# Kernel optimization log

Measured on AMD Instinct MI355X. Metric: run time of the kernel, lower is better.

## Reference

```python
import jax, jax.numpy as jnp
import numpy as np

B, T, C = 2, 2048, 1024
NH = 16
HD = C // NH

def build_alibi_bias(n_head, max_len):
    slopes = jnp.arange(1, n_head + 1, dtype=jnp.float32) / n_head  # [nh]
    ar = jnp.arange(max_len, dtype=jnp.float32)
    # bias[h, i, j] = slopes[h] * (j - i)
    return slopes[:, None, None] * (ar[None, None, :] - ar[None, :, None])

def setup_inputs() -> dict:
    key = jax.random.key(0)
    ks = jax.random.split(key, 7)
    s = 0.02
    return {
        "x": jax.random.normal(ks[0], (B, T, C), dtype=jnp.float32),
        "q_w": jax.random.normal(ks[1], (C, C), dtype=jnp.float32) * s,   # [in, out]
        "q_b": jnp.zeros((C,), dtype=jnp.float32),
        "kv_w": jax.random.normal(ks[2], (C, 2 * C), dtype=jnp.float32) * s,
        "kv_b": jnp.zeros((2 * C,), dtype=jnp.float32),
        "o_w": jax.random.normal(ks[3], (C, C), dtype=jnp.float32) * s,
        "o_b": jnp.zeros((C,), dtype=jnp.float32),
    }

def reference(x, q_w, q_b, kv_w, kv_b, o_w, o_b):
    Bx, Tx, Cx = x.shape
    q = (x @ q_w + q_b).reshape(Bx, Tx, NH, HD).transpose(0, 2, 1, 3)      # [B,nh,T,hd]
    kv = (x @ kv_w + kv_b).reshape(Bx, Tx, 2, NH, HD).transpose(2, 0, 3, 1, 4)
    k, v = kv[0], kv[1]                                                     # [B,nh,T,hd]
    att = jnp.einsum("bhqd,bhkd->bhqk", q, k) * (1.0 / np.sqrt(HD))        # [B,nh,T,T]
    att = att + build_alibi_bias(NH, Tx)[None]                              # ALiBi bias
    causal = jnp.tril(jnp.ones((Tx, Tx), dtype=bool))
    att = jnp.where(causal[None, None], att, -jnp.inf)
    att = jax.nn.softmax(att, axis=-1)
    y = jnp.einsum("bhqk,bhkd->bhqd", att, v)                               # [B,nh,T,hd]
    y = y.transpose(0, 2, 1, 3).reshape(Bx, Tx, Cx)
    return y @ o_w + o_b
```

## Files before the change

kernel.cpp:

```cpp
#include <hip/hip_runtime.h>
#include <hip/hip_bf16.h>

#define NB 2
#define NT 2048
#define NC 1024
#define NHD 16
#define HDD 64
#define LOG2E 1.4426950408889634f

typedef __attribute__((ext_vector_type(8))) short short8;
typedef __attribute__((ext_vector_type(4))) short short4v;
typedef __attribute__((ext_vector_type(4))) float f32x4;
typedef __attribute__((ext_vector_type(16))) float f32x16;

__device__ __forceinline__ ushort f2bf(float f) {
    union { float f; unsigned u; } v; v.f = f;
    unsigned u = v.u;
    unsigned r = (u + 0x7FFFu + ((u >> 16) & 1u)) >> 16;
    return (ushort)r;
}

__device__ __forceinline__ float bf2f(ushort u) {
    unsigned x = ((unsigned)u) << 16;
    float f; __builtin_memcpy(&f, &x, 4); return f;
}

__device__ __forceinline__ unsigned pkbf(float a, float b) {
    __hip_bfloat162 t = __float22bfloat162_rn(float2{a, b});
    unsigned u; __builtin_memcpy(&u, &t, 4); return u;
}

__device__ __forceinline__ void gload16(const ushort* g, ushort* l) {
    __builtin_amdgcn_global_load_lds((const __attribute__((address_space(1))) void*)g,
                                     (__attribute__((address_space(3))) void*)l, 16, 0, 0);
}

__device__ __forceinline__ void tcvt_tile(const float* __restrict__ src, ushort* __restrict__ dst,
                                          int Kd, int Nd, int kb, int nb)
{
    __shared__ ushort tile[64][68];
    const int tid = threadIdx.x;
    const int r = tid >> 2, c = (tid & 3) * 16;
    const float* sp = src + (size_t)(kb + r) * Nd + nb + c;
#pragma unroll
    for (int i = 0; i < 16; i += 4) {
        float4 v = *(const float4*)(sp + i);
        tile[r][c + i + 0] = f2bf(v.x);
        tile[r][c + i + 1] = f2bf(v.y);
        tile[r][c + i + 2] = f2bf(v.z);
        tile[r][c + i + 3] = f2bf(v.w);
    }
    __syncthreads();
    ushort* dp = dst + (size_t)(nb + r) * Kd + kb + c;
#pragma unroll
    for (int i = 0; i < 16; i += 8) {
        short8 o;
#pragma unroll
        for (int j = 0; j < 8; j++) o[j] = (short)tile[c + i + j][r];
        *(short8*)(dp + i) = o;
    }
}

__global__ __launch_bounds__(256)
void prep(const float* __restrict__ x, const float* __restrict__ q_w,
          const float* __restrict__ kv_w, const float* __restrict__ o_w,
          ushort* __restrict__ xb, ushort* __restrict__ wqkvT, ushort* __restrict__ woT)
{
    const int bid = blockIdx.x;
    if (bid < 2048) {
        int i = (bid * 256 + threadIdx.x) * 8;
        float4 a = *(const float4*)(x + i);
        float4 b = *(const float4*)(x + i + 4);
        short8 o;
        o[0] = (short)f2bf(a.x); o[1] = (short)f2bf(a.y);
        o[2] = (short)f2bf(a.z); o[3] = (short)f2bf(a.w);
        o[4] = (short)f2bf(b.x); o[5] = (short)f2bf(b.y);
        o[6] = (short)f2bf(b.z); o[7] = (short)f2bf(b.w);
        *(short8*)(xb + i) = o;
    } else if (bid < 2304) {
        int r = bid - 2048;
        tcvt_tile(q_w, wqkvT, 1024, 1024, (r & 15) * 64, (r >> 4) * 64);
    } else if (bid < 2816) {
        int r = bid - 2304;
        tcvt_tile(kv_w, wqkvT + 1024 * 1024, 1024, 2048, (r & 15) * 64, (r >> 4) * 64);
    } else {
        int r = bid - 2816;
        tcvt_tile(o_w, woT, 1024, 1024, (r & 15) * 64, (r >> 4) * 64);
    }
}

template<int MODE>
__global__ __launch_bounds__(256)
void gemm128(const ushort* __restrict__ A, const ushort* __restrict__ Bt,
             const float* __restrict__ bias0, const float* __restrict__ bias1,
             ushort* __restrict__ Qo, ushort* __restrict__ Ko, ushort* __restrict__ VoT,
             float* __restrict__ Fo, int Kdim)
{
    __shared__ ushort Al[2][128 * 32];
    __shared__ ushort Bl[2][128 * 32];
    const int tid = threadIdx.x;
    const int lane = tid & 63, w = tid >> 6;
    const int wr = (w >> 1) * 64, wc = (w & 1) * 64;
    const int lg = lane >> 4, lc = lane & 15;

    const int nwg = gridDim.x;
    const int cpx = nwg >> 3;
    const int sid = (blockIdx.x & 7) * cpx + (blockIdx.x >> 3);
    const int bm = (sid & 31) * 128, bn = (sid >> 5) * 128;

    f32x4 acc[4][4] = {};

    const int srow = lane >> 2, scol = (lane & 3) * 8;
    const int seg0 = w * 2;

    const ushort* apb = A  + (size_t)(bm + seg0 * 16 + srow) * Kdim + scol;
    const ushort* bpb = Bt + (size_t)(bn + seg0 * 16 + srow) * Kdim + scol;

    gload16(apb,              &Al[0][seg0 * 512]);
    gload16(apb + 16 * Kdim,  &Al[0][(seg0 + 1) * 512]);
    gload16(bpb,              &Bl[0][seg0 * 512]);
    gload16(bpb + 16 * Kdim,  &Bl[0][(seg0 + 1) * 512]);

    int cur = 0;
    for (int k0 = 0; k0 < Kdim; k0 += 32) {
        __syncthreads();
        if (k0 + 32 < Kdim) {
            gload16(apb + (k0 + 32),             &Al[cur ^ 1][seg0 * 512]);
            gload16(apb + (k0 + 32) + 16 * Kdim, &Al[cur ^ 1][(seg0 + 1) * 512]);
            gload16(bpb + (k0 + 32),             &Bl[cur ^ 1][seg0 * 512]);
            gload16(bpb + (k0 + 32) + 16 * Kdim, &Bl[cur ^ 1][(seg0 + 1) * 512]);
        }
        short8 af[4], bfv[4];
#pragma unroll
        for (int mt = 0; mt < 4; mt++) af[mt] = *(const short8*)&Al[cur][(wr + mt*16 + lc) * 32 + lg*8];
#pragma unroll
        for (int nt = 0; nt < 4; nt++) bfv[nt] = *(const short8*)&Bl[cur][(wc + nt*16 + lc) * 32 + lg*8];
        __builtin_amdgcn_s_setprio(1);
#pragma unroll
        for (int mt = 0; mt < 4; mt++)
#pragma unroll
            for (int nt = 0; nt < 4; nt++)
                acc[mt][nt] = __builtin_amdgcn_mfma_f32_16x16x32_bf16(af[mt], bfv[nt], acc[mt][nt], 0, 0, 0);
        __builtin_amdgcn_s_setprio(0);
        cur ^= 1;
    }

#pragma unroll
    for (int mt = 0; mt < 4; mt++) {
#pragma unroll
        for (int nt = 0; nt < 4; nt++) {
            const int n = bn + wc + nt * 16 + lc;
            const int mb = bm + wr + mt * 16 + lg * 4;
            if (MODE == 1) {
#pragma unroll
                for (int rr = 0; rr < 4; rr++)
                    Fo[(size_t)(mb + rr) * NC + n] = acc[mt][nt][rr] + bias0[n];
            } else {
                const int b = mb >> 11, t = mb & 2047;
                const int reg = n >> 10;
                if (reg == 0) {
                    int hh = n >> 6, d = n & 63;
                    ushort* qp = Qo + (((size_t)b * NHD + hh) * NT + t) * HDD + d;
#pragma unroll
                    for (int rr = 0; rr < 4; rr++)
                        qp[rr * HDD] = f2bf((acc[mt][nt][rr] + bias0[n]) * (0.125f * LOG2E));
                } else if (reg == 1) {
                    int j = n - NC;
                    int hh = j >> 6, d = j & 63;
                    ushort* kp = Ko + (((size_t)b * NHD + hh) * NT + t) * HDD + d;
#pragma unroll
                    for (int rr = 0; rr < 4; rr++)
                        kp[rr * HDD] = f2bf(acc[mt][nt][rr] + bias1[j]);
                } else {
                    int j = n - NC;
                    int jj = j - 1024;
                    int hh = jj >> 6, d = jj & 63;
                    short4v o;
#pragma unroll
                    for (int rr = 0; rr < 4; rr++)
                        o[rr] = (short)f2bf(acc[mt][nt][rr] + bias1[j]);
                    *(short4v*)&VoT[(((size_t)b * NHD + hh) * HDD + d) * NT + t] = o;
                }
            }
        }
    }
}

__global__ __launch_bounds__(256, 3)
void attn_fwd(const ushort* __restrict__ Q, const ushort* __restrict__ K,
              const ushort* __restrict__ Vt, ushort* __restrict__ Y,
              ushort* __restrict__ pool0, ushort* __restrict__ pool1,
              float* __restrict__ mlb)
{
    __shared__ ushort sb[2 * 2 * 64 * 72];

    const int tid = threadIdx.x;
    const int lane = tid & 63, w = tid >> 6;
    const int lo5 = lane & 31, hi = lane >> 5;
    const int slot = (int)(blockIdx.x >> 5);
    const int bh = blockIdx.x & 31;
    const int b = bh >> 4, h = bh & 15;

    int qt, seg, nseg;
    if (slot < 16)      { qt = 15 - (slot >> 2); seg = slot & 3; nseg = 4; }
    else if (slot < 28) { int u = slot - 16; int q3 = u / 3; qt = 11 - q3; seg = u - q3 * 3; nseg = 3; }
    else if (slot < 36) { int u = slot - 28; qt = 7 - (u >> 1); seg = u & 1; nseg = 2; }
    else                { qt = 39 - slot; seg = 0; nseg = 1; }
    const int T = 2 * qt + 2;
    const int t_begin = (seg * T) / nseg;
    const int t_end   = ((seg + 1) * T) / nseg;
    const bool split = (nseg > 1);
    int pi = 0;
    if (split) {
        int pbase = (qt < 8) ? (qt - 4) * 2 : ((qt < 12) ? 8 + (qt - 8) * 3 : 20 + (qt - 12) * 4);
        pi = bh * 36 + pbase + seg;
    }

    const ushort* Qp = Q + (size_t)bh * NT * HDD;
    const ushort* Kp = K + (size_t)bh * NT * HDD;
    const ushort* Vp = Vt + (size_t)bh * HDD * NT;

    const int q0 = qt * 128 + w * 32;
    const int qlane = q0 + lo5;

    const float slope2 = (float)(h + 1) * (LOG2E / (float)NHD);

    short8 qf[4];
    {
        const ushort* qr = Qp + (size_t)qlane * HDD + 8 * hi;
#pragma unroll
        for (int kk = 0; kk < 4; kk++) qf[kk] = *(const short8*)(qr + kk * 16);
    }

    short8 ones;
#pragma unroll
    for (int j = 0; j < 8; j++) ones[j] = (short)0x3F80;

    float bb[16];
#pragma unroll
    for (int r = 0; r < 16; r++) {
        int roff = (r & 3) + 8 * (r >> 2) + 4 * hi;
        bb[r] = slope2 * ((float)roff - (float)qlane);
    }

    float m_s = -1e30f, l_s = 0.f;
    f32x16 accO[2] = {};

    const int sr = tid >> 2, sd = (tid & 3) * 16;

    short8 pk0, pk1, pv0, pv1;
    {
        const ushort* kp = Kp + (size_t)(t_begin * 64 + sr) * HDD + sd;
        pk0 = *(const short8*)kp;
        pk1 = *(const short8*)(kp + 8);
        const ushort* vp = Vp + (size_t)sr * NT + t_begin * 64 + sd;
        pv0 = *(const short8*)vp;
        pv1 = *(const short8*)(vp + 8);
    }

    for (int t = t_begin; t < t_end; t++) {
        const int kv0 = t * 64;
        ushort* Kl = sb + ((t - t_begin) & 1) * 2 * 64 * 72;
        ushort* Vl = Kl + 64 * 72;
        *(short8*)&Kl[sr * 72 + sd]     = pk0;
        *(short8*)&Kl[sr * 72 + sd + 8] = pk1;
        *(short8*)&Vl[sr * 72 + sd]     = pv0;
        *(short8*)&Vl[sr * 72 + sd + 8] = pv1;
        __syncthreads();

        if (t + 1 < t_end) {
            const int kv1 = kv0 + 64;
            const ushort* kp = Kp + (size_t)(kv1 + sr) * HDD + sd;
            pk0 = *(const short8*)kp;
            pk1 = *(const short8*)(kp + 8);
            const ushort* vp = Vp + (size_t)sr * NT + kv1 + sd;
            pv0 = *(const short8*)vp;
            pv1 = *(const short8*)(vp + 8);
        }

#pragma unroll
        for (int sub = 0; sub < 2; sub++) {
            const int kv0s = kv0 + sub * 32;
            if (kv0s > q0 + 31) continue;

            f32x16 S = {};
            __builtin_amdgcn_s_setprio(1);
#pragma unroll
            for (int kk = 0; kk < 4; kk++) {
                short8 kf = *(const short8*)&Kl[(sub * 32 + lo5) * 72 + kk * 16 + 8 * hi];
                S = __builtin_amdgcn_mfma_f32_32x32x16_bf16(kf, qf[kk], S, 0, 0, 0);
            }
            __builtin_amdgcn_s_setprio(0);

            const float sk = slope2 * (float)kv0s;
            float mloc = m_s - sk;

            if (kv0s + 31 > q0) {
#pragma unroll
                for (int r = 0; r < 16; r++) {
                    int kvr = kv0s + (r & 3) + 8 * (r >> 2) + 4 * hi;
                    S[r] = (kvr > qlane) ? -1e30f : (S[r] + bb[r]);
                }
            } else {
#pragma unroll
                for (int r = 0; r < 16; r++) S[r] = S[r] + bb[r];
            }

            float a0 = fmaxf(fmaxf(S[0], S[1]), S[2]);
            float a1 = fmaxf(fmaxf(S[3], S[4]), S[5]);
            float a2 = fmaxf(fmaxf(S[6], S[7]), S[8]);
            float a3 = fmaxf(fmaxf(S[9], S[10]), S[11]);
            float a4 = fmaxf(fmaxf(S[12], S[13]), S[14]);
            float rmax = fmaxf(fmaxf(fmaxf(a0, a1), fmaxf(a2, a3)), fmaxf(a4, S[15]));
            rmax = fmaxf(rmax, __shfl_xor(rmax, 32));

            if (__any(rmax - mloc > 8.0f)) {
                float mn = fmaxf(mloc, rmax);
                float sc = __builtin_amdgcn_exp2f(mloc - mn);
                mloc = mn;
                l_s *= sc;
#pragma unroll
                for (int dt = 0; dt < 2; dt++)
#pragma unroll
                    for (int r = 0; r < 16; r++) accO[dt][r] *= sc;
            }
            m_s = mloc + sk;

#pragma unroll
            for (int r = 0; r < 16; r++)
                S[r] = __builtin_amdgcn_exp2f(S[r] - mloc);

            unsigned pw[8];
#pragma unroll
            for (int i = 0; i < 8; i++) pw[i] = pkbf(S[2 * i], S[2 * i + 1]);
            asm volatile("v_permlane32_swap_b32 %0, %1" : "+v"(pw[0]), "+v"(pw[2]));
            asm volatile("v_permlane32_swap_b32 %0, %1" : "+v"(pw[1]), "+v"(pw[3]));
            asm volatile("v_permlane32_swap_b32 %0, %1" : "+v"(pw[4]), "+v"(pw[6]));
            asm volatile("v_permlane32_swap_b32 %0, %1" : "+v"(pw[5]), "+v"(pw[7]));
            union { unsigned u[4]; short8 s; } fa0, fa1;
            fa0.u[0] = pw[0]; fa0.u[1] = pw[1]; fa0.u[2] = pw[2]; fa0.u[3] = pw[3];
            fa1.u[0] = pw[4]; fa1.u[1] = pw[5]; fa1.u[2] = pw[6]; fa1.u[3] = pw[7];

            f32x16 z = {};
            __builtin_amdgcn_s_setprio(1);
            z = __builtin_amdgcn_mfma_f32_32x32x16_bf16(ones, fa0.s, z, 0, 0, 0);
            z = __builtin_amdgcn_mfma_f32_32x32x16_bf16(ones, fa1.s, z, 0, 0, 0);

#pragma unroll
            for (int dt = 0; dt < 2; dt++) {
                short8 vf0 = *(const short8*)&Vl[(dt * 32 + lo5) * 72 + sub * 32 + 8 * hi];
                short8 vf1 = *(const short8*)&Vl[(dt * 32 + lo5) * 72 + sub * 32 + 16 + 8 * hi];
                accO[dt] = __builtin_amdgcn_mfma_f32_32x32x16_bf16(vf0, fa0.s, accO[dt], 0, 0, 0);
                accO[dt] = __builtin_amdgcn_mfma_f32_32x32x16_bf16(vf1, fa1.s, accO[dt], 0, 0, 0);
            }
            __builtin_amdgcn_s_setprio(0);

            l_s += z[0];
        }
    }

    const float invl = split ? 1.0f : __builtin_amdgcn_rcpf(l_s);
    __syncthreads();
    ushort* myO = sb + w * 32 * 72;
#pragma unroll
    for (int dt = 0; dt < 2; dt++)
#pragma unroll
        for (int r = 0; r < 16; r++) {
            int d = dt * 32 + (r & 3) + 8 * (r >> 2) + 4 * hi;
            myO[lo5 * 72 + d] = f2bf(accO[dt][r] * invl);
        }
    if (split && hi == 0) {
        int rowin = w * 32 + lo5;
        mlb[pi * 256 + rowin] = m_s;
        mlb[pi * 256 + 128 + rowin] = l_s;
    }
    __syncthreads();
    const int orow = lane >> 1, ocol = (lane & 1) * 32;
    if (split) {
        ushort* pp = (pi < 320 ? pool0 + (size_t)pi * 8192 : pool1 + (size_t)(pi - 320) * 8192)
                     + (w * 32 + orow) * 64 + ocol;
#pragma unroll
        for (int c = 0; c < 4; c++)
            *(short8*)(pp + c * 8) = *(const short8*)&myO[orow * 72 + ocol + c * 8];
    } else {
        ushort* yp = Y + ((size_t)b * NT + q0 + orow) * NC + h * HDD + ocol;
#pragma unroll
        for (int c = 0; c < 4; c++)
            *(short8*)(yp + c * 8) = *(const short8*)&myO[orow * 72 + ocol + c * 8];
    }
}

__global__ __launch_bounds__(256)
void combine(const ushort* __restrict__ pool0, const ushort* __restrict__ pool1,
             const float* __restrict__ mlb, ushort* __restrict__ Y)
{
    const int cb = blockIdx.x;
    const int bh = cb / 12, qs = cb % 12;
    const int qt = qs + 4;
    const int b = bh >> 4, h = bh & 15;
    const int nseg = (qs < 4) ? 2 : ((qs < 8) ? 3 : 4);
    const int pbase = (qs < 4) ? qs * 2 : ((qs < 8) ? 8 + (qs - 4) * 3 : 20 + (qs - 8) * 4);
    const int pi0 = bh * 36 + pbase;

    const int tid = threadIdx.x;
    const int r = tid >> 1, c0 = (tid & 1) * 32;

    float m[4], l[4], a[4];
    float M = -1e30f;
    for (int s = 0; s < nseg; s++) {
        m[s] = mlb[(pi0 + s) * 256 + r];
        l[s] = mlb[(pi0 + s) * 256 + 128 + r];
        M = fmaxf(M, m[s]);
    }
    float L = 0.f;
    for (int s = 0; s < nseg; s++) { a[s] = __builtin_amdgcn_exp2f(m[s] - M); L += a[s] * l[s]; }
    const float inv = __builtin_amdgcn_rcpf(L);

    const ushort* pp[4];
    for (int s = 0; s < nseg; s++) {
        int pi = pi0 + s;
        pp[s] = (pi < 320 ? pool0 + (size_t)pi * 8192 : pool1 + (size_t)(pi - 320) * 8192) + r * 64 + c0;
    }
    ushort* yp = Y + ((size_t)b * NT + qt * 128 + r) * NC + h * HDD + c0;

#pragma unroll
    for (int c = 0; c < 4; c++) {
        float acc[8] = {};
        for (int s = 0; s < nseg; s++) {
            short8 u = *(const short8*)(pp[s] + c * 8);
#pragma unroll
            for (int j = 0; j < 8; j++) acc[j] += a[s] * bf2f((ushort)u[j]);
        }
        short8 o;
#pragma unroll
        for (int j = 0; j < 8; j++) o[j] = (short)f2bf(acc[j] * inv);
        *(short8*)(yp + c * 8) = o;
    }
}

extern "C" void kernel_launch(void* const* d_in, const int* in_sizes, int n_in,
                              void* d_out, int out_size, void* d_ws, size_t ws_size,
                              hipStream_t stream)
{
    const float* x    = (const float*)d_in[0];
    const float* q_w  = (const float*)d_in[1];
    const float* q_b  = (const float*)d_in[2];
    const float* kv_w = (const float*)d_in[3];
    const float* kv_b = (const float*)d_in[4];
    const float* o_w  = (const float*)d_in[5];
    const float* o_b  = (const float*)d_in[6];
    float* out = (float*)d_out;

    char* ws = (char*)d_ws;
    ushort* xb    = (ushort*)(ws);
    ushort* wqkvT = (ushort*)(ws + 8388608);
    ushort* woT   = (ushort*)(ws + 14680064);
    ushort* Qs    = (ushort*)(ws + 16777216);
    ushort* Ks    = (ushort*)(ws + 25165824);
    ushort* VsT   = (ushort*)(ws + 33554432);
    ushort* Ys    = (ushort*)(ws + 41943040);
    ushort* pool0 = wqkvT;
    ushort* pool1 = (ushort*)out;
    float*  mlb   = (float*)((char*)out + 832 * 16384);

    prep<<<3072, 256, 0, stream>>>(x, q_w, kv_w, o_w, xb, wqkvT, woT);
    gemm128<0><<<768, 256, 0, stream>>>(xb, wqkvT, q_b, kv_b, Qs, Ks, VsT, nullptr, 1024);
    attn_fwd<<<1280, 256, 0, stream>>>(Qs, Ks, VsT, Ys, pool0, pool1, mlb);
    combine<<<384, 256, 0, stream>>>(pool0, pool1, mlb, Ys);
    gemm128<1><<<256, 256, 0, stream>>>(Ys, woT, o_b, nullptr, nullptr, nullptr, nullptr, out, 1024);
}
```

Measured before the change: 132.3 us.

## Process two 32-row query tiles per wave to double K/V LDS reuse

Each wave now handles 64 query rows (two 32-row Q fragments with separate online-softmax state), so every block covers a 256-row query chunk and K/V tiles staged in LDS are reused twice as much. The split-KV scheduling, partial pool layout, m/l buffer layout and combine kernel are all rewritten for 256-row chunks, and the grid shrinks to 640 attention blocks and 192 combine blocks. This cuts global K/V traffic and loop overhead per query row, but raises register pressure from doubled accumulators and Q fragments, and leaves fewer blocks to spread across CUs.

```diff
diff --git a/kernel.cpp b/kernel.cpp
--- a/kernel.cpp
+++ b/kernel.cpp
@@ -186,6 +186,87 @@
     }
 }
 
+__device__ __forceinline__ void qtile_step(
+    const ushort* Kl, const ushort* Vl, int sub,
+    const short8* qf, const float* bb, short8 ones,
+    float slope2, int kv0s, int q0t, int qlt, int lo5, int hi,
+    float& m_s, float& l_s, f32x16* accO)
+{
+    f32x16 S = {};
+    __builtin_amdgcn_s_setprio(1);
+#pragma unroll
+    for (int kk = 0; kk < 4; kk++) {
+        short8 kf = *(const short8*)&Kl[(sub * 32 + lo5) * 72 + kk * 16 + 8 * hi];
+        S = __builtin_amdgcn_mfma_f32_32x32x16_bf16(kf, qf[kk], S, 0, 0, 0);
+    }
+    __builtin_amdgcn_s_setprio(0);
+
+    const float sk = slope2 * (float)kv0s;
+    float mloc = m_s - sk;
+
+    if (kv0s + 31 > q0t) {
+#pragma unroll
+        for (int r = 0; r < 16; r++) {
+            int kvr = kv0s + (r & 3) + 8 * (r >> 2) + 4 * hi;
+            S[r] = (kvr > qlt) ? -1e30f : (S[r] + bb[r]);
+        }
+    } else {
+#pragma unroll
+        for (int r = 0; r < 16; r++) S[r] = S[r] + bb[r];
+    }
+
+    float a0 = fmaxf(fmaxf(S[0], S[1]), S[2]);
+    float a1 = fmaxf(fmaxf(S[3], S[4]), S[5]);
+    float a2 = fmaxf(fmaxf(S[6], S[7]), S[8]);
+    float a3 = fmaxf(fmaxf(S[9], S[10]), S[11]);
+    float a4 = fmaxf(fmaxf(S[12], S[13]), S[14]);
+    float rmax = fmaxf(fmaxf(fmaxf(a0, a1), fmaxf(a2, a3)), fmaxf(a4, S[15]));
+    rmax = fmaxf(rmax, __shfl_xor(rmax, 32));
+
+    if (__any(rmax - mloc > 8.0f)) {
+        float mn = fmaxf(mloc, rmax);
+        float sc = __builtin_amdgcn_exp2f(mloc - mn);
+        mloc = mn;
+        l_s *= sc;
+#pragma unroll
+        for (int dt = 0; dt < 2; dt++)
+#pragma unroll
+            for (int r = 0; r < 16; r++) accO[dt][r] *= sc;
+    }
+    m_s = mloc + sk;
+
+#pragma unroll
+    for (int r = 0; r < 16; r++)
+        S[r] = __builtin_amdgcn_exp2f(S[r] - mloc);
+
+    unsigned pw[8];
+#pragma unroll
+    for (int i = 0; i < 8; i++) pw[i] = pkbf(S[2 * i], S[2 * i + 1]);
+    asm volatile("v_permlane32_swap_b32 %0, %1" : "+v"(pw[0]), "+v"(pw[2]));
+    asm volatile("v_permlane32_swap_b32 %0, %1" : "+v"(pw[1]), "+v"(pw[3]));
+    asm volatile("v_permlane32_swap_b32 %0, %1" : "+v"(pw[4]), "+v"(pw[6]));
+    asm volatile("v_permlane32_swap_b32 %0, %1" : "+v"(pw[5]), "+v"(pw[7]));
+    union { unsigned u[4]; short8 s; } fa0, fa1;
+    fa0.u[0] = pw[0]; fa0.u[1] = pw[1]; fa0.u[2] = pw[2]; fa0.u[3] = pw[3];
+    fa1.u[0] = pw[4]; fa1.u[1] = pw[5]; fa1.u[2] = pw[6]; fa1.u[3] = pw[7];
+
+    f32x16 z = {};
+    __builtin_amdgcn_s_setprio(1);
+    z = __builtin_amdgcn_mfma_f32_32x32x16_bf16(ones, fa0.s, z, 0, 0, 0);
+    z = __builtin_amdgcn_mfma_f32_32x32x16_bf16(ones, fa1.s, z, 0, 0, 0);
+
+#pragma unroll
+    for (int dt = 0; dt < 2; dt++) {
+        short8 vf0 = *(const short8*)&Vl[(dt * 32 + lo5) * 72 + sub * 32 + 8 * hi];
+        short8 vf1 = *(const short8*)&Vl[(dt * 32 + lo5) * 72 + sub * 32 + 16 + 8 * hi];
+        accO[dt] = __builtin_amdgcn_mfma_f32_32x32x16_bf16(vf0, fa0.s, accO[dt], 0, 0, 0);
+        accO[dt] = __builtin_amdgcn_mfma_f32_32x32x16_bf16(vf1, fa1.s, accO[dt], 0, 0, 0);
+    }
+    __builtin_amdgcn_s_setprio(0);
+
+    l_s += z[0];
+}
+
 __global__ __launch_bounds__(256, 3)
 void attn_fwd(const ushort* __restrict__ Q, const ushort* __restrict__ K,
               const ushort* __restrict__ Vt, ushort* __restrict__ Y,
@@ -201,35 +282,38 @@
     const int bh = blockIdx.x & 31;
     const int b = bh >> 4, h = bh & 15;
 
-    int qt, seg, nseg;
-    if (slot < 16)      { qt = 15 - (slot >> 2); seg = slot & 3; nseg = 4; }
-    else if (slot < 28) { int u = slot - 16; int q3 = u / 3; qt = 11 - q3; seg = u - q3 * 3; nseg = 3; }
-    else if (slot < 36) { int u = slot - 28; qt = 7 - (u >> 1); seg = u & 1; nseg = 2; }
-    else                { qt = 39 - slot; seg = 0; nseg = 1; }
-    const int T = 2 * qt + 2;
+    int qc, seg, nseg;
+    if (slot < 8)       { qc = 7 - (slot >> 2); seg = slot & 3; nseg = 4; }
+    else if (slot < 14) { int u = slot - 8; int q3 = u / 3; qc = 5 - q3; seg = u - q3 * 3; nseg = 3; }
+    else if (slot < 18) { int u = slot - 14; qc = 3 - (u >> 1); seg = u & 1; nseg = 2; }
+    else                { qc = 19 - slot; seg = 0; nseg = 1; }
+    const int T = 4 * qc + 4;
     const int t_begin = (seg * T) / nseg;
     const int t_end   = ((seg + 1) * T) / nseg;
     const bool split = (nseg > 1);
     int pi = 0;
     if (split) {
-        int pbase = (qt < 8) ? (qt - 4) * 2 : ((qt < 12) ? 8 + (qt - 8) * 3 : 20 + (qt - 12) * 4);
-        pi = bh * 36 + pbase + seg;
+        int pbase = (qc == 7) ? 0 : (qc == 6) ? 4 : (qc == 5) ? 8 : (qc == 4) ? 11 : (qc == 3) ? 14 : 16;
+        pi = bh * 18 + pbase + seg;
     }
 
     const ushort* Qp = Q + (size_t)bh * NT * HDD;
     const ushort* Kp = K + (size_t)bh * NT * HDD;
     const ushort* Vp = Vt + (size_t)bh * HDD * NT;
 
-    const int q0 = qt * 128 + w * 32;
-    const int qlane = q0 + lo5;
+    const int q0w = qc * 256 + w * 64;
+    const int qlA = q0w + lo5;
 
     const float slope2 = (float)(h + 1) * (LOG2E / (float)NHD);
 
-    short8 qf[4];
+    short8 qfA[4], qfB[4];
     {
-        const ushort* qr = Qp + (size_t)qlane * HDD + 8 * hi;
-#pragma unroll
-        for (int kk = 0; kk < 4; kk++) qf[kk] = *(const short8*)(qr + kk * 16);
+        const ushort* qr = Qp + (size_t)qlA * HDD + 8 * hi;
+#pragma unroll
+        for (int kk = 0; kk < 4; kk++) qfA[kk] = *(const short8*)(qr + kk * 16);
+        const ushort* qr2 = qr + 32 * HDD;
+#pragma unroll
+        for (int kk = 0; kk < 4; kk++) qfB[kk] = *(const short8*)(qr2 + kk * 16);
     }
 
     short8 ones;
@@ -240,11 +324,11 @@
 #pragma unroll
     for (int r = 0; r < 16; r++) {
         int roff = (r & 3) + 8 * (r >> 2) + 4 * hi;
-        bb[r] = slope2 * ((float)roff - (float)qlane);
-    }
-
-    float m_s = -1e30f, l_s = 0.f;
-    f32x16 accO[2] = {};
+        bb[r] = slope2 * (float)roff;
+    }
+
+    float m_a = -1e30f, l_a = 0.f, m_b = -1e30f, l_b = 0.f;
+    f32x16 accA[2] = {}, accB[2] = {};
 
     const int sr = tid >> 2, sd = (tid & 3) * 16;
 
@@ -281,112 +365,52 @@
 #pragma unroll
         for (int sub = 0; sub < 2; sub++) {
             const int kv0s = kv0 + sub * 32;
-            if (kv0s > q0 + 31) continue;
-
-            f32x16 S = {};
-            __builtin_amdgcn_s_setprio(1);
-#pragma unroll
-            for (int kk = 0; kk < 4; kk++) {
-                short8 kf = *(const short8*)&Kl[(sub * 32 + lo5) * 72 + kk * 16 + 8 * hi];
-                S = __builtin_amdgcn_mfma_f32_32x32x16_bf16(kf, qf[kk], S, 0, 0, 0);
-            }
-            __builtin_amdgcn_s_setprio(0);
-
-            const float sk = slope2 * (float)kv0s;
-            float mloc = m_s - sk;
-
-            if (kv0s + 31 > q0) {
-#pragma unroll
-                for (int r = 0; r < 16; r++) {
-                    int kvr = kv0s + (r & 3) + 8 * (r >> 2) + 4 * hi;
-                    S[r] = (kvr > qlane) ? -1e30f : (S[r] + bb[r]);
-                }
-            } else {
-#pragma unroll
-                for (int r = 0; r < 16; r++) S[r] = S[r] + bb[r];
-            }
-
-            float a0 = fmaxf(fmaxf(S[0], S[1]), S[2]);
-            float a1 = fmaxf(fmaxf(S[3], S[4]), S[5]);
-            float a2 = fmaxf(fmaxf(S[6], S[7]), S[8]);
-            float a3 = fmaxf(fmaxf(S[9], S[10]), S[11]);
-            float a4 = fmaxf(fmaxf(S[12], S[13]), S[14]);
-            float rmax = fmaxf(fmaxf(fmaxf(a0, a1), fmaxf(a2, a3)), fmaxf(a4, S[15]));
-            rmax = fmaxf(rmax, __shfl_xor(rmax, 32));
-
-            if (__any(rmax - mloc > 8.0f)) {
-                float mn = fmaxf(mloc, rmax);
-                float sc = __builtin_amdgcn_exp2f(mloc - mn);
-                mloc = mn;
-                l_s *= sc;
-#pragma unroll
-                for (int dt = 0; dt < 2; dt++)
-#pragma unroll
-                    for (int r = 0; r < 16; r++) accO[dt][r] *= sc;
-            }
-            m_s = mloc + sk;
-
-#pragma unroll
-            for (int r = 0; r < 16; r++)
-                S[r] = __builtin_amdgcn_exp2f(S[r] - mloc);
-
-            unsigned pw[8];
-#pragma unroll
-            for (int i = 0; i < 8; i++) pw[i] = pkbf(S[2 * i], S[2 * i + 1]);
-            asm volatile("v_permlane32_swap_b32 %0, %1" : "+v"(pw[0]), "+v"(pw[2]));
-            asm volatile("v_permlane32_swap_b32 %0, %1" : "+v"(pw[1]), "+v"(pw[3]));
-            asm volatile("v_permlane32_swap_b32 %0, %1" : "+v"(pw[4]), "+v"(pw[6]));
-            asm volatile("v_permlane32_swap_b32 %0, %1" : "+v"(pw[5]), "+v"(pw[7]));
-            union { unsigned u[4]; short8 s; } fa0, fa1;
-            fa0.u[0] = pw[0]; fa0.u[1] = pw[1]; fa0.u[2] = pw[2]; fa0.u[3] = pw[3];
-            fa1.u[0] = pw[4]; fa1.u[1] = pw[5]; fa1.u[2] = pw[6]; fa1.u[3] = pw[7];
-
-            f32x16 z = {};
-            __builtin_amdgcn_s_setprio(1);
-            z = __builtin_amdgcn_mfma_f32_32x32x16_bf16(ones, fa0.s, z, 0, 0, 0);
-            z = __builtin_amdgcn_mfma_f32_32x32x16_bf16(ones, fa1.s, z, 0, 0, 0);
-
-#pragma unroll
-            for (int dt = 0; dt < 2; dt++) {
-                short8 vf0 = *(const short8*)&Vl[(dt * 32 + lo5) * 72 + sub * 32 + 8 * hi];
-                short8 vf1 = *(const short8*)&Vl[(dt * 32 + lo5) * 72 + sub * 32 + 16 + 8 * hi];
-                accO[dt] = __builtin_amdgcn_mfma_f32_32x32x16_bf16(vf0, fa0.s, accO[dt], 0, 0, 0);
-                accO[dt] = __builtin_amdgcn_mfma_f32_32x32x16_bf16(vf1, fa1.s, accO[dt], 0, 0, 0);
-            }
-            __builtin_amdgcn_s_setprio(0);
-
-            l_s += z[0];
-        }
-    }
-
-    const float invl = split ? 1.0f : __builtin_amdgcn_rcpf(l_s);
+            if (kv0s > q0w + 63) continue;
+            if (kv0s <= q0w + 31)
+                qtile_step(Kl, Vl, sub, qfA, bb, ones, slope2, kv0s,
+                           q0w, qlA, lo5, hi, m_a, l_a, accA);
+            qtile_step(Kl, Vl, sub, qfB, bb, ones, slope2, kv0s,
+                       q0w + 32, qlA + 32, lo5, hi, m_b, l_b, accB);
+        }
+    }
+
+    const float invA = split ? 1.0f : __builtin_amdgcn_rcpf(l_a);
+    const float invB = split ? 1.0f : __builtin_amdgcn_rcpf(l_b);
     __syncthreads();
-    ushort* myO = sb + w * 32 * 72;
+    ushort* myO = sb + w * 64 * 72;
 #pragma unroll
     for (int dt = 0; dt < 2; dt++)
 #pragma unroll
         for (int r = 0; r < 16; r++) {
             int d = dt * 32 + (r & 3) + 8 * (r >> 2) + 4 * hi;
-            myO[lo5 * 72 + d] = f2bf(accO[dt][r] * invl);
+            myO[lo5 * 72 + d]        = f2bf(accA[dt][r] * invA);
+            myO[(32 + lo5) * 72 + d] = f2bf(accB[dt][r] * invB);
         }
     if (split && hi == 0) {
-        int rowin = w * 32 + lo5;
-        mlb[pi * 256 + rowin] = m_s;
-        mlb[pi * 256 + 128 + rowin] = l_s;
+        int base = pi * 512 + w * 64 + lo5;
+        mlb[base]            = m_a;
+        mlb[base + 32]       = m_b;
+        mlb[base + 256]      = l_a;
+        mlb[base + 256 + 32] = l_b;
     }
     __syncthreads();
     const int orow = lane >> 1, ocol = (lane & 1) * 32;
-    if (split) {
-        ushort* pp = (pi < 320 ? pool0 + (size_t)pi * 8192 : pool1 + (size_t)(pi - 320) * 8192)
-                     + (w * 32 + orow) * 64 + ocol;
-#pragma unroll
-        for (int c = 0; c < 4; c++)
-            *(short8*)(pp + c * 8) = *(const short8*)&myO[orow * 72 + ocol + c * 8];
-    } else {
-        ushort* yp = Y + ((size_t)b * NT + q0 + orow) * NC + h * HDD + ocol;
-#pragma unroll
-        for (int c = 0; c < 4; c++)
-            *(short8*)(yp + c * 8) = *(const short8*)&myO[orow * 72 + ocol + c * 8];
+#pragma unroll
+    for (int ro = 0; ro < 2; ro++) {
+        const int row = ro * 32 + orow;
+        if (split) {
+            ushort* pp = (pi < 192 ? pool0 + (size_t)pi * 16384
+                                   : pool1 + (size_t)(pi - 192) * 16384)
+                         + (w * 64 + row) * 64 + ocol;
+#pragma unroll
+            for (int c = 0; c < 4; c++)
+                *(short8*)(pp + c * 8) = *(const short8*)&myO[row * 72 + ocol + c * 8];
+        } else {
+            ushort* yp = Y + ((size_t)b * NT + q0w + row) * NC + h * HDD + ocol;
+#pragma unroll
+            for (int c = 0; c < 4; c++)
+                *(short8*)(yp + c * 8) = *(const short8*)&myO[row * 72 + ocol + c * 8];
+        }
     }
 }
 
@@ -395,21 +419,20 @@
              const float* __restrict__ mlb, ushort* __restrict__ Y)
 {
     const int cb = blockIdx.x;
-    const int bh = cb / 12, qs = cb % 12;
-    const int qt = qs + 4;
+    const int bh = cb / 6, qs = cb % 6;
+    const int qc = 7 - qs;
     const int b = bh >> 4, h = bh & 15;
-    const int nseg = (qs < 4) ? 2 : ((qs < 8) ? 3 : 4);
-    const int pbase = (qs < 4) ? qs * 2 : ((qs < 8) ? 8 + (qs - 4) * 3 : 20 + (qs - 8) * 4);
-    const int pi0 = bh * 36 + pbase;
-
-    const int tid = threadIdx.x;
-    const int r = tid >> 1, c0 = (tid & 1) * 32;
+    const int nseg = (qs < 2) ? 4 : (qs < 4) ? 3 : 2;
+    const int pbase = (qs == 0) ? 0 : (qs == 1) ? 4 : (qs == 2) ? 8 : (qs == 3) ? 11 : (qs == 4) ? 14 : 16;
+    const int pi0 = bh * 18 + pbase;
+
+    const int r = threadIdx.x;
 
     float m[4], l[4], a[4];
     float M = -1e30f;
     for (int s = 0; s < nseg; s++) {
-        m[s] = mlb[(pi0 + s) * 256 + r];
-        l[s] = mlb[(pi0 + s) * 256 + 128 + r];
+        m[s] = mlb[(pi0 + s) * 512 + r];
+        l[s] = mlb[(pi0 + s) * 512 + 256 + r];
         M = fmaxf(M, m[s]);
     }
     float L = 0.f;
@@ -419,12 +442,12 @@
     const ushort* pp[4];
     for (int s = 0; s < nseg; s++) {
         int pi = pi0 + s;
-        pp[s] = (pi < 320 ? pool0 + (size_t)pi * 8192 : pool1 + (size_t)(pi - 320) * 8192) + r * 64 + c0;
-    }
-    ushort* yp = Y + ((size_t)b * NT + qt * 128 + r) * NC + h * HDD + c0;
-
-#pragma unroll
-    for (int c = 0; c < 4; c++) {
+        pp[s] = (pi < 192 ? pool0 + (size_t)pi * 16384 : pool1 + (size_t)(pi - 192) * 16384) + r * 64;
+    }
+    ushort* yp = Y + ((size_t)b * NT + qc * 256 + r) * NC + h * HDD;
+
+#pragma unroll
+    for (int c = 0; c < 8; c++) {
         float acc[8] = {};
         for (int s = 0; s < nseg; s++) {
             short8 u = *(const short8*)(pp[s] + c * 8);
@@ -461,11 +484,11 @@
     ushort* Ys    = (ushort*)(ws + 41943040);
     ushort* pool0 = wqkvT;
     ushort* pool1 = (ushort*)out;
-    float*  mlb   = (float*)((char*)out + 832 * 16384);
+    float*  mlb   = (float*)((char*)out + 12582912);
 
     prep<<<3072, 256, 0, stream>>>(x, q_w, kv_w, o_w, xb, wqkvT, woT);
     gemm128<0><<<768, 256, 0, stream>>>(xb, wqkvT, q_b, kv_b, Qs, Ks, VsT, nullptr, 1024);
-    attn_fwd<<<1280, 256, 0, stream>>>(Qs, Ks, VsT, Ys, pool0, pool1, mlb);
-    combine<<<384, 256, 0, stream>>>(pool0, pool1, mlb, Ys);
+    attn_fwd<<<640, 256, 0, stream>>>(Qs, Ks, VsT, Ys, pool0, pool1, mlb);
+    combine<<<192, 256, 0, stream>>>(pool0, pool1, mlb, Ys);
     gemm128<1><<<256, 256, 0, stream>>>(Ys, woT, o_b, nullptr, nullptr, nullptr, nullptr, out, 1024);
 }
```

Result: slower. 171.8 us (+29.8%).

## Enlarge attention query tile to 256 rows with 8 waves sharing K/V tiles

Applied to the files above, without the earlier changes.

The attention kernel now runs 512-thread blocks covering 256 query rows instead of 128, so each staged 64-row K/V tile in shared memory serves twice as many waves. That halves global K/V traffic per query and halves the per-thread staging loads. The split-K schedule, partial-result pool indexing, m/l buffer layout and the combine kernel are all rebuilt for the coarser chunks. The costs are coarser causal load balance, idle waves waiting at barriers on diagonal tiles, fewer blocks, and a dropped occupancy hint in the launch bounds.

```diff
diff --git a/kernel.cpp b/kernel.cpp
--- a/kernel.cpp
+++ b/kernel.cpp
@@ -186,7 +186,7 @@
     }
 }
 
-__global__ __launch_bounds__(256, 3)
+__global__ __launch_bounds__(512)
 void attn_fwd(const ushort* __restrict__ Q, const ushort* __restrict__ K,
               const ushort* __restrict__ Vt, ushort* __restrict__ Y,
               ushort* __restrict__ pool0, ushort* __restrict__ pool1,
@@ -201,26 +201,26 @@
     const int bh = blockIdx.x & 31;
     const int b = bh >> 4, h = bh & 15;
 
-    int qt, seg, nseg;
-    if (slot < 16)      { qt = 15 - (slot >> 2); seg = slot & 3; nseg = 4; }
-    else if (slot < 28) { int u = slot - 16; int q3 = u / 3; qt = 11 - q3; seg = u - q3 * 3; nseg = 3; }
-    else if (slot < 36) { int u = slot - 28; qt = 7 - (u >> 1); seg = u & 1; nseg = 2; }
-    else                { qt = 39 - slot; seg = 0; nseg = 1; }
-    const int T = 2 * qt + 2;
+    int qc, seg, nseg;
+    if (slot < 8)       { qc = 7 - (slot >> 2); seg = slot & 3; nseg = 4; }
+    else if (slot < 14) { int u = slot - 8; int q3 = u / 3; qc = 5 - q3; seg = u - q3 * 3; nseg = 3; }
+    else if (slot < 18) { int u = slot - 14; qc = 3 - (u >> 1); seg = u & 1; nseg = 2; }
+    else                { qc = 19 - slot; seg = 0; nseg = 1; }
+    const int T = 4 * qc + 4;
     const int t_begin = (seg * T) / nseg;
     const int t_end   = ((seg + 1) * T) / nseg;
     const bool split = (nseg > 1);
     int pi = 0;
     if (split) {
-        int pbase = (qt < 8) ? (qt - 4) * 2 : ((qt < 12) ? 8 + (qt - 8) * 3 : 20 + (qt - 12) * 4);
-        pi = bh * 36 + pbase + seg;
+        int pbase = (qc == 7) ? 0 : (qc == 6) ? 4 : (qc == 5) ? 8 : (qc == 4) ? 11 : (qc == 3) ? 14 : 16;
+        pi = bh * 18 + pbase + seg;
     }
 
     const ushort* Qp = Q + (size_t)bh * NT * HDD;
     const ushort* Kp = K + (size_t)bh * NT * HDD;
     const ushort* Vp = Vt + (size_t)bh * HDD * NT;
 
-    const int q0 = qt * 128 + w * 32;
+    const int q0 = qc * 256 + w * 32;
     const int qlane = q0 + lo5;
 
     const float slope2 = (float)(h + 1) * (LOG2E / (float)NHD);
@@ -246,36 +246,26 @@
     float m_s = -1e30f, l_s = 0.f;
     f32x16 accO[2] = {};
 
-    const int sr = tid >> 2, sd = (tid & 3) * 16;
-
-    short8 pk0, pk1, pv0, pv1;
+    const int sr = tid >> 3, sd = (tid & 7) * 8;
+
+    short8 pk, pv;
     {
-        const ushort* kp = Kp + (size_t)(t_begin * 64 + sr) * HDD + sd;
-        pk0 = *(const short8*)kp;
-        pk1 = *(const short8*)(kp + 8);
-        const ushort* vp = Vp + (size_t)sr * NT + t_begin * 64 + sd;
-        pv0 = *(const short8*)vp;
-        pv1 = *(const short8*)(vp + 8);
+        pk = *(const short8*)(Kp + (size_t)(t_begin * 64 + sr) * HDD + sd);
+        pv = *(const short8*)(Vp + (size_t)sr * NT + t_begin * 64 + sd);
     }
 
     for (int t = t_begin; t < t_end; t++) {
         const int kv0 = t * 64;
         ushort* Kl = sb + ((t - t_begin) & 1) * 2 * 64 * 72;
         ushort* Vl = Kl + 64 * 72;
-        *(short8*)&Kl[sr * 72 + sd]     = pk0;
-        *(short8*)&Kl[sr * 72 + sd + 8] = pk1;
-        *(short8*)&Vl[sr * 72 + sd]     = pv0;
-        *(short8*)&Vl[sr * 72 + sd + 8] = pv1;
+        *(short8*)&Kl[sr * 72 + sd] = pk;
+        *(short8*)&Vl[sr * 72 + sd] = pv;
         __syncthreads();
 
         if (t + 1 < t_end) {
             const int kv1 = kv0 + 64;
-            const ushort* kp = Kp + (size_t)(kv1 + sr) * HDD + sd;
-            pk0 = *(const short8*)kp;
-            pk1 = *(const short8*)(kp + 8);
-            const ushort* vp = Vp + (size_t)sr * NT + kv1 + sd;
-            pv0 = *(const short8*)vp;
-            pv1 = *(const short8*)(vp + 8);
+            pk = *(const short8*)(Kp + (size_t)(kv1 + sr) * HDD + sd);
+            pv = *(const short8*)(Vp + (size_t)sr * NT + kv1 + sd);
         }
 
 #pragma unroll
@@ -371,14 +361,16 @@
         }
     if (split && hi == 0) {
         int rowin = w * 32 + lo5;
-        mlb[pi * 256 + rowin] = m_s;
-        mlb[pi * 256 + 128 + rowin] = l_s;
+        mlb[pi * 512 + rowin]       = m_s;
+        mlb[pi * 512 + 256 + rowin] = l_s;
     }
     __syncthreads();
     const int orow = lane >> 1, ocol = (lane & 1) * 32;
+    const int row = w * 32 + orow;
     if (split) {
-        ushort* pp = (pi < 320 ? pool0 + (size_t)pi * 8192 : pool1 + (size_t)(pi - 320) * 8192)
-                     + (w * 32 + orow) * 64 + ocol;
+        ushort* pp = (pi < 192 ? pool0 + (size_t)pi * 16384
+                               : pool1 + (size_t)(pi - 192) * 16384)
+                     + row * 64 + ocol;
 #pragma unroll
         for (int c = 0; c < 4; c++)
             *(short8*)(pp + c * 8) = *(const short8*)&myO[orow * 72 + ocol + c * 8];
@@ -395,21 +387,20 @@
              const float* __restrict__ mlb, ushort* __restrict__ Y)
 {
     const int cb = blockIdx.x;
-    const int bh = cb / 12, qs = cb % 12;
-    const int qt = qs + 4;
+    const int bh = cb / 6, qs = cb % 6;
+    const int qc = 7 - qs;
     const int b = bh >> 4, h = bh & 15;
-    const int nseg = (qs < 4) ? 2 : ((qs < 8) ? 3 : 4);
-    const int pbase = (qs < 4) ? qs * 2 : ((qs < 8) ? 8 + (qs - 4) * 3 : 20 + (qs - 8) * 4);
-    const int pi0 = bh * 36 + pbase;
-
-    const int tid = threadIdx.x;
-    const int r = tid >> 1, c0 = (tid & 1) * 32;
+    const int nseg = (qs < 2) ? 4 : (qs < 4) ? 3 : 2;
+    const int pbase = (qs == 0) ? 0 : (qs == 1) ? 4 : (qs == 2) ? 8 : (qs == 3) ? 11 : (qs == 4) ? 14 : 16;
+    const int pi0 = bh * 18 + pbase;
+
+    const int r = threadIdx.x;
 
     float m[4], l[4], a[4];
     float M = -1e30f;
     for (int s = 0; s < nseg; s++) {
-        m[s] = mlb[(pi0 + s) * 256 + r];
-        l[s] = mlb[(pi0 + s) * 256 + 128 + r];
+        m[s] = mlb[(pi0 + s) * 512 + r];
+        l[s] = mlb[(pi0 + s) * 512 + 256 + r];
         M = fmaxf(M, m[s]);
     }
     float L = 0.f;
@@ -419,12 +410,12 @@
     const ushort* pp[4];
     for (int s = 0; s < nseg; s++) {
         int pi = pi0 + s;
-        pp[s] = (pi < 320 ? pool0 + (size_t)pi * 8192 : pool1 + (size_t)(pi - 320) * 8192) + r * 64 + c0;
-    }
-    ushort* yp = Y + ((size_t)b * NT + qt * 128 + r) * NC + h * HDD + c0;
-
-#pragma unroll
-    for (int c = 0; c < 4; c++) {
+        pp[s] = (pi < 192 ? pool0 + (size_t)pi * 16384 : pool1 + (size_t)(pi - 192) * 16384) + r * 64;
+    }
+    ushort* yp = Y + ((size_t)b * NT + qc * 256 + r) * NC + h * HDD;
+
+#pragma unroll
+    for (int c = 0; c < 8; c++) {
         float acc[8] = {};
         for (int s = 0; s < nseg; s++) {
             short8 u = *(const short8*)(pp[s] + c * 8);
@@ -461,11 +452,11 @@
     ushort* Ys    = (ushort*)(ws + 41943040);
     ushort* pool0 = wqkvT;
     ushort* pool1 = (ushort*)out;
-    float*  mlb   = (float*)((char*)out + 832 * 16384);
+    float*  mlb   = (float*)((char*)out + 12582912);
 
     prep<<<3072, 256, 0, stream>>>(x, q_w, kv_w, o_w, xb, wqkvT, woT);
     gemm128<0><<<768, 256, 0, stream>>>(xb, wqkvT, q_b, kv_b, Qs, Ks, VsT, nullptr, 1024);
-    attn_fwd<<<1280, 256, 0, stream>>>(Qs, Ks, VsT, Ys, pool0, pool1, mlb);
-    combine<<<384, 256, 0, stream>>>(pool0, pool1, mlb, Ys);
+    attn_fwd<<<640, 512, 0, stream>>>(Qs, Ks, VsT, Ys, pool0, pool1, mlb);
+    combine<<<192, 256, 0, stream>>>(pool0, pool1, mlb, Ys);
     gemm128<1><<<256, 256, 0, stream>>>(Ys, woT, o_b, nullptr, nullptr, nullptr, nullptr, out, 1024);
 }
```

Measured after the change: 147.5 us. 1.11x slower.
